# Performance work log

Measured on AMD Instinct MI355X. Metric: run time of the kernel, lower is better.

## Reference

```python
import jax, jax.numpy as jnp
import numpy as np

M, K, N = 8192, 1024, 8192

def setup_inputs() -> dict:
    key = jax.random.key(0)
    k1, k2, k3, k4 = jax.random.split(key, 4)
    # a, b are int8-valued quantized tensors (stored as int32 per harness dtype set)
    a = jax.random.randint(k1, (M, K), 0, 127, dtype=jnp.int32)
    b = jax.random.randint(k2, (K, N), 0, 127, dtype=jnp.int32)
    alpha_row = jax.random.uniform(k3, (M, 1), dtype=jnp.float32)
    alpha_col = jax.random.uniform(k4, (1, N), dtype=jnp.float32)
    return {"a": a, "b": b, "alpha_row": alpha_row, "alpha_col": alpha_col}

def reference(a, b, alpha_row, alpha_col):
    # Faithful to TorchGemmA8W8.forward: upcast int8 operands to fp32,
    # matmul with fp32 accumulate, cast result to int8.
    # (alpha_row / alpha_col are accepted but unused in this variant.)
    x = jnp.matmul(a.astype(jnp.float32), b.astype(jnp.float32))  # [M, N] fp32
    return x.astype(jnp.int8)
```

## Files before the change

kernel.cpp:

```cpp
#include <hip/hip_runtime.h>
#include <stdint.h>

#define M_DIM 8192
#define N_DIM 8192
#define K_DIM 1024
#define BK    128

typedef int int4v __attribute__((ext_vector_type(4)));

__device__ __forceinline__ void gload16(const char* g, char* l) {
    __builtin_amdgcn_global_load_lds(
        (__attribute__((address_space(1))) void*)(void*)const_cast<char*>(g),
        (__attribute__((address_space(3))) void*)l,
        16, 0, 0);
}

__device__ __forceinline__ int sat8(int v) {
    v = v > 127 ? 127 : v;
    v = v < -128 ? -128 : v;
    return v;
}

__global__ __launch_bounds__(256) void pack_ab_kernel(const int* __restrict__ a,
                                                      const int* __restrict__ b,
                                                      char* __restrict__ outA,
                                                      char* __restrict__ outB) {
    __shared__ char tile[64][68];
    const int t = threadIdx.x;
    if (blockIdx.x < 8192) {
        const int m   = blockIdx.x;
        const int row = m & 127;
        const int xr  = (row >> 1) & 3;
        const int4 v  = ((const int4*)a)[m * 256 + t];
        const int pk  = (v.x & 0xff) | ((v.y & 0xff) << 8) |
                        ((v.z & 0xff) << 16) | ((v.w & 0xff) << 24);
        const int k     = t * 4;
        const int slice = k >> 6;
        const int sc    = ((k >> 4) & 3) ^ xr;
        *(int*)&outA[(size_t)(m >> 7) * 131072 + slice * 8192 + row * 64 +
                     sc * 16 + (k & 15)] = pk;
        return;
    }
    const int bx = blockIdx.x - 8192;
    const int n0 = (bx & 127) * 64;
    const int k0 = (bx >> 7) * 64;
    const int tr  = t >> 4;
    const int tc4 = (t & 15) << 2;
#pragma unroll
    for (int j = 0; j < 4; ++j) {
        int row = tr + j * 16;
        int4 v = *(const int4*)&b[(size_t)(k0 + row) * N_DIM + n0 + tc4];
        tile[row][tc4 + 0] = (char)v.x;
        tile[row][tc4 + 1] = (char)v.y;
        tile[row][tc4 + 2] = (char)v.z;
        tile[row][tc4 + 3] = (char)v.w;
    }
    __syncthreads();
    const int slice = k0 >> 6;
#pragma unroll
    for (int j = 0; j < 4; ++j) {
        int n = tr + j * 16;
        int pk = (tile[tc4 + 0][n] & 0xff) |
                 ((tile[tc4 + 1][n] & 0xff) << 8) |
                 ((tile[tc4 + 2][n] & 0xff) << 16) |
                 ((tile[tc4 + 3][n] & 0xff) << 24);
        const int ng  = n0 + n;
        const int row = ng & 127;
        const int sc  = (tc4 >> 4) ^ ((row >> 1) & 3);
        *(int*)&outB[(size_t)(ng >> 7) * 131072 + slice * 8192 + row * 64 +
                     sc * 16 + (tc4 & 15)] = pk;
    }
}

__global__ __launch_bounds__(256) void gemm_i8_kernel(const char* __restrict__ A8,
                                                      const char* __restrict__ B8,
                                                      int* __restrict__ C) {
    __shared__ __align__(16) char smem[4 * 8704];
    char* As = smem;
    char* Bs = smem + 16384;

    const int t    = threadIdx.x;
    const int xcd  = blockIdx.x & 7;
    const int j    = blockIdx.x >> 3;
    const int bm   = (xcd << 3) | (j & 7);
    const int bn   = j >> 3;
    const int lane = t & 63;
    const int wave = t >> 6;
    const int wm   = wave >> 1;
    const int wn   = wave & 1;
    const int quad = lane >> 4;
    const int l16  = lane & 15;

    const char* aT = A8 + (size_t)bm * 131072;
    const char* bT = B8 + (size_t)bn * 131072;

    const int laneByte = ((quad ^ ((l16 >> 1) & 3)) << 4);

    int4v acc[4][4] = {};

    for (int kt = 0; kt < K_DIM / BK; ++kt) {
        const size_t kBase = (size_t)kt * 16384;
#pragma unroll
        for (int s = 0; s < 4; ++s) {
            const int f = s * 4096 + t * 16;
            gload16(aT + kBase + f, As + f);
            gload16(bT + kBase + f, Bs + f);
        }
        __syncthreads();

#pragma unroll
        for (int h = 0; h < 2; ++h) {
            int4v af[4], bf[4];
#pragma unroll
            for (int mi = 0; mi < 4; ++mi)
                af[mi] = *(const int4v*)
                    &As[h * 8192 + (wm * 64 + mi * 16 + l16) * 64 + laneByte];
#pragma unroll
            for (int ni = 0; ni < 4; ++ni)
                bf[ni] = *(const int4v*)
                    &Bs[h * 8192 + (wn * 64 + ni * 16 + l16) * 64 + laneByte];

#pragma unroll
            for (int mi = 0; mi < 4; ++mi)
#pragma unroll
                for (int ni = 0; ni < 4; ++ni)
                    acc[mi][ni] = __builtin_amdgcn_mfma_i32_16x16x64_i8(
                        af[mi], bf[ni], acc[mi][ni], 0, 0, 0);
        }

        __syncthreads();
    }

    int* lw = (int*)(smem + wave * 8704);
    const int mW = bm * 128 + wm * 64;
    const int nW = bn * 128 + wn * 64;
#pragma unroll
    for (int rnd = 0; rnd < 2; ++rnd) {
#pragma unroll
        for (int mh = 0; mh < 2; ++mh) {
            const int mi = rnd * 2 + mh;
#pragma unroll
            for (int ni = 0; ni < 4; ++ni)
#pragma unroll
                for (int r = 0; r < 4; ++r)
                    lw[(mh * 16 + quad * 4 + r) * 68 + ni * 16 + l16] =
                        sat8(acc[mi][ni][r]);
        }
#pragma unroll
        for (int rr = 0; rr < 8; ++rr) {
            const int R = rr * 4 + quad;
            const int4v v = *(const int4v*)&lw[R * 68 + l16 * 4];
            *(int4v*)&C[(size_t)(mW + rnd * 32 + R) * N_DIM + nW + l16 * 4] = v;
        }
    }
}

__global__ __launch_bounds__(256) void gemm_naive_kernel(const int* __restrict__ a,
                                                         const int* __restrict__ b,
                                                         int* __restrict__ C) {
    const int col = blockIdx.x * 256 + threadIdx.x;
    const int row = blockIdx.y;
    int acc = 0;
    for (int k = 0; k < K_DIM; ++k)
        acc += a[(size_t)row * K_DIM + k] * b[(size_t)k * N_DIM + col];
    C[(size_t)row * N_DIM + col] = sat8(acc);
}

extern "C" void kernel_launch(void* const* d_in, const int* in_sizes, int n_in,
                              void* d_out, int out_size, void* d_ws, size_t ws_size,
                              hipStream_t stream) {
    const int* a = (const int*)d_in[0];
    const int* b = (const int*)d_in[1];
    int* out = (int*)d_out;

    const size_t needed = 2 * (size_t)M_DIM * K_DIM;
    if (ws_size < needed) {
        gemm_naive_kernel<<<dim3(N_DIM / 256, M_DIM), 256, 0, stream>>>(a, b, out);
        return;
    }

    char* A8 = (char*)d_ws;
    char* B8 = A8 + (size_t)M_DIM * K_DIM;

    pack_ab_kernel<<<8192 + 2048, 256, 0, stream>>>(a, b, A8, B8);
    gemm_i8_kernel<<<4096, 256, 0, stream>>>(A8, B8, out);
}
```

Baseline: 366.7 us.

## Use 256x256 tiles with a four-slot LDS ring and phase-interleaved prefetch

The int8 GEMM kernel moves from 128x128 tiles with 256 threads to 256x256 tiles with 512 threads, so each wave computes a 128x64 output block and reuses more data per LDS load. Staging becomes a four-slot ring of 64-deep k slices. Each MFMA phase issues one async global-to-LDS copy for a later slice, guarded by explicit barriers, waitcnt and setprio, so global loads overlap compute instead of stalling on a sync per k tile. In exchange, the kernel uses 128 KB of LDS (about one block per CU), drops the XCD-aware block remapping, and carries many more accumulator registers.

```diff
diff --git a/kernel.cpp b/kernel.cpp
--- a/kernel.cpp
+++ b/kernel.cpp
@@ -4,7 +4,6 @@
 #define M_DIM 8192
 #define N_DIM 8192
 #define K_DIM 1024
-#define BK    128
 
 typedef int int4v __attribute__((ext_vector_type(4)));
 
@@ -72,70 +71,103 @@
     }
 }
 
-__global__ __launch_bounds__(256) void gemm_i8_kernel(const char* __restrict__ A8,
-                                                      const char* __restrict__ B8,
-                                                      int* __restrict__ C) {
-    __shared__ __align__(16) char smem[4 * 8704];
-    char* As = smem;
-    char* Bs = smem + 16384;
+__global__ __launch_bounds__(512, 2) void gemm_i8_kernel(const char* __restrict__ A8,
+                                                         const char* __restrict__ B8,
+                                                         int* __restrict__ C) {
+    __shared__ __align__(16) char smem[131072];
 
     const int t    = threadIdx.x;
-    const int xcd  = blockIdx.x & 7;
-    const int j    = blockIdx.x >> 3;
-    const int bm   = (xcd << 3) | (j & 7);
-    const int bn   = j >> 3;
+    const int bn   = blockIdx.x;
+    const int bm   = blockIdx.y;
     const int lane = t & 63;
     const int wave = t >> 6;
-    const int wm   = wave >> 1;
-    const int wn   = wave & 1;
+    const int wm   = wave >> 2;
+    const int wn   = wave & 3;
     const int quad = lane >> 4;
     const int l16  = lane & 15;
-
-    const char* aT = A8 + (size_t)bm * 131072;
-    const char* bT = B8 + (size_t)bn * 131072;
+    const int f16  = t * 16;
+
+    const char* aT0 = A8 + (size_t)(2 * bm) * 131072;
+    const char* aT1 = aT0 + 131072;
+    const char* bT0 = B8 + (size_t)(2 * bn) * 131072;
+    const char* bT1 = bT0 + 131072;
 
     const int laneByte = ((quad ^ ((l16 >> 1) & 3)) << 4);
-
-    int4v acc[4][4] = {};
-
-    for (int kt = 0; kt < K_DIM / BK; ++kt) {
-        const size_t kBase = (size_t)kt * 16384;
-#pragma unroll
-        for (int s = 0; s < 4; ++s) {
-            const int f = s * 4096 + t * 16;
-            gload16(aT + kBase + f, As + f);
-            gload16(bT + kBase + f, Bs + f);
-        }
-        __syncthreads();
-
-#pragma unroll
-        for (int h = 0; h < 2; ++h) {
-            int4v af[4], bf[4];
-#pragma unroll
-            for (int mi = 0; mi < 4; ++mi)
-                af[mi] = *(const int4v*)
-                    &As[h * 8192 + (wm * 64 + mi * 16 + l16) * 64 + laneByte];
-#pragma unroll
-            for (int ni = 0; ni < 4; ++ni)
-                bf[ni] = *(const int4v*)
-                    &Bs[h * 8192 + (wn * 64 + ni * 16 + l16) * 64 + laneByte];
-
-#pragma unroll
-            for (int mi = 0; mi < 4; ++mi)
-#pragma unroll
-                for (int ni = 0; ni < 4; ++ni)
-                    acc[mi][ni] = __builtin_amdgcn_mfma_i32_16x16x64_i8(
-                        af[mi], bf[ni], acc[mi][ni], 0, 0, 0);
-        }
-
-        __syncthreads();
-    }
+    const int aRowByte = (wm * 128 + l16) * 64 + laneByte;
+    const int bRowByte = (wn * 64 + l16) * 64 + laneByte;
+
+    int4v acc[8][4] = {};
+    int4v bf[4];
+
+#define STG_A0(T,S) gload16(aT0 + (T)*8192 + f16, smem + (S)*16384 + f16)
+#define STG_A1(T,S) gload16(aT1 + (T)*8192 + f16, smem + (S)*16384 + 8192 + f16)
+#define STG_B0(T,S) gload16(bT0 + (T)*8192 + f16, smem + 65536 + (S)*16384 + f16)
+#define STG_B1(T,S) gload16(bT1 + (T)*8192 + f16, smem + 65536 + (S)*16384 + 8192 + f16)
+
+#define PHASE(SLOT, MIH, LOADB, STG, VMW) do {                                      \
+    int4v af0 = *(const int4v*)&smem[(SLOT)*16384 + aRowByte + ((MIH)*2+0)*1024];   \
+    int4v af1 = *(const int4v*)&smem[(SLOT)*16384 + aRowByte + ((MIH)*2+1)*1024];   \
+    if (LOADB) {                                                                    \
+        bf[0] = *(const int4v*)&smem[65536 + (SLOT)*16384 + bRowByte + 0*1024];     \
+        bf[1] = *(const int4v*)&smem[65536 + (SLOT)*16384 + bRowByte + 1*1024];     \
+        bf[2] = *(const int4v*)&smem[65536 + (SLOT)*16384 + bRowByte + 2*1024];     \
+        bf[3] = *(const int4v*)&smem[65536 + (SLOT)*16384 + bRowByte + 3*1024];     \
+    }                                                                               \
+    STG;                                                                            \
+    __builtin_amdgcn_s_barrier();                                                   \
+    asm volatile("s_waitcnt lgkmcnt(0)" ::: "memory");                              \
+    __builtin_amdgcn_sched_barrier(0);                                 \
+    __builtin_amdgcn_s_setprio(1);                                                  \
+    _Pragma("unroll")                                                               \
+    for (int ni = 0; ni < 4; ++ni) {                                                \
+        acc[(MIH)*2+0][ni] = __builtin_amdgcn_mfma_i32_16x16x64_i8(                 \
+            af0, bf[ni], acc[(MIH)*2+0][ni], 0, 0, 0);                              \
+        acc[(MIH)*2+1][ni] = __builtin_amdgcn_mfma_i32_16x16x64_i8(                 \
+            af1, bf[ni], acc[(MIH)*2+1][ni], 0, 0, 0);                              \
+    }                                                                               \
+    __builtin_amdgcn_s_setprio(0);                                                  \
+    if (VMW) asm volatile("s_waitcnt vmcnt(4)" ::: "memory");                       \
+    __builtin_amdgcn_s_barrier();                                                   \
+} while (0)
+
+    STG_A0(0, 0); STG_A1(0, 0); STG_B0(0, 0); STG_B1(0, 0);
+    STG_A0(1, 1); STG_A1(1, 1); STG_B0(1, 1); STG_B1(1, 1);
+    asm volatile("s_waitcnt vmcnt(4)" ::: "memory");
+    __builtin_amdgcn_s_barrier();
+    __builtin_amdgcn_sched_barrier(0);
+
+#pragma unroll 2
+    for (int j = 0; j < 8; ++j) {
+        const int s0 = (2 * j) & 3;
+        const int s1 = (2 * j + 1) & 3;
+        const int su0 = (2 * j + 2) & 3;
+        const int su1 = (2 * j + 3) & 3;
+        const int u0 = (j < 7) ? 2 * j + 2 : 15;
+        const int u1 = (j < 7) ? 2 * j + 3 : 15;
+
+        PHASE(s0, 0, 1, STG_A0(u0, su0), 0);
+        PHASE(s0, 1, 0, STG_A1(u0, su0), 0);
+        PHASE(s0, 2, 0, STG_B0(u0, su0), 0);
+        PHASE(s0, 3, 0, STG_B1(u0, su0), 1);
+        PHASE(s1, 0, 1, STG_A0(u1, su1), 0);
+        PHASE(s1, 1, 0, STG_A1(u1, su1), 0);
+        PHASE(s1, 2, 0, STG_B0(u1, su1), 0);
+        PHASE(s1, 3, 0, STG_B1(u1, su1), 1);
+    }
+#undef PHASE
+#undef STG_A0
+#undef STG_A1
+#undef STG_B0
+#undef STG_B1
+
+    asm volatile("s_waitcnt vmcnt(0)" ::: "memory");
+    __builtin_amdgcn_s_barrier();
 
     int* lw = (int*)(smem + wave * 8704);
-    const int mW = bm * 128 + wm * 64;
-    const int nW = bn * 128 + wn * 64;
-#pragma unroll
-    for (int rnd = 0; rnd < 2; ++rnd) {
+    const int mBase = bm * 256 + wm * 128;
+    const int nW    = bn * 256 + wn * 64;
+#pragma unroll
+    for (int rnd = 0; rnd < 4; ++rnd) {
 #pragma unroll
         for (int mh = 0; mh < 2; ++mh) {
             const int mi = rnd * 2 + mh;
@@ -150,7 +182,7 @@
         for (int rr = 0; rr < 8; ++rr) {
             const int R = rr * 4 + quad;
             const int4v v = *(const int4v*)&lw[R * 68 + l16 * 4];
-            *(int4v*)&C[(size_t)(mW + rnd * 32 + R) * N_DIM + nW + l16 * 4] = v;
+            *(int4v*)&C[(size_t)(mBase + rnd * 32 + R) * N_DIM + nW + l16 * 4] = v;
         }
     }
 }
@@ -183,5 +215,5 @@
     char* B8 = A8 + (size_t)M_DIM * K_DIM;
 
     pack_ab_kernel<<<8192 + 2048, 256, 0, stream>>>(a, b, A8, B8);
-    gemm_i8_kernel<<<4096, 256, 0, stream>>>(A8, B8, out);
-}
+    gemm_i8_kernel<<<dim3(N_DIM / 256, M_DIM / 256), 512, 0, stream>>>(A8, B8, out);
+}
```

Measured after the change: 367.8 us. No clear change (+0.3%).

## Give each wave private double-buffered LDS tiles and drop block barriers

Applied to the files above, without the earlier changes.

The shared block-wide tile load with two __syncthreads per K step is replaced by per-wave private LDS regions. Each wave streams only its own 64-row A and B slices through a two-deep buffer using global_load_lds, synchronising with explicit vmcnt/lgkmcnt waits and raising priority around the MFMA block. This removes the barriers and overlaps the global loads with compute. The cost is redundant global traffic, since waves sharing a row or column each fetch the same slice, and the tail re-issues dummy loads of the last slice.

```diff
diff --git a/kernel.cpp b/kernel.cpp
--- a/kernel.cpp
+++ b/kernel.cpp
@@ -4,7 +4,6 @@
 #define M_DIM 8192
 #define N_DIM 8192
 #define K_DIM 1024
-#define BK    128
 
 typedef int int4v __attribute__((ext_vector_type(4)));
 
@@ -75,9 +74,7 @@
 __global__ __launch_bounds__(256) void gemm_i8_kernel(const char* __restrict__ A8,
                                                       const char* __restrict__ B8,
                                                       int* __restrict__ C) {
-    __shared__ __align__(16) char smem[4 * 8704];
-    char* As = smem;
-    char* Bs = smem + 16384;
+    __shared__ __align__(16) char smem[4][16384];
 
     const int t    = threadIdx.x;
     const int xcd  = blockIdx.x & 7;
@@ -90,48 +87,71 @@
     const int wn   = wave & 1;
     const int quad = lane >> 4;
     const int l16  = lane & 15;
-
-    const char* aT = A8 + (size_t)bm * 131072;
-    const char* bT = B8 + (size_t)bn * 131072;
+    const int lb   = lane * 16;
+
+    char* myA = &smem[wave][0];
+    char* myB = &smem[wave][8192];
+
+    const char* aW = A8 + (size_t)bm * 131072 + wm * 4096;
+    const char* bW = B8 + (size_t)bn * 131072 + wn * 4096;
 
     const int laneByte = ((quad ^ ((l16 >> 1) & 3)) << 4);
 
     int4v acc[4][4] = {};
 
-    for (int kt = 0; kt < K_DIM / BK; ++kt) {
-        const size_t kBase = (size_t)kt * 16384;
-#pragma unroll
-        for (int s = 0; s < 4; ++s) {
-            const int f = s * 4096 + t * 16;
-            gload16(aT + kBase + f, As + f);
-            gload16(bT + kBase + f, Bs + f);
-        }
-        __syncthreads();
-
-#pragma unroll
-        for (int h = 0; h < 2; ++h) {
-            int4v af[4], bf[4];
-#pragma unroll
-            for (int mi = 0; mi < 4; ++mi)
-                af[mi] = *(const int4v*)
-                    &As[h * 8192 + (wm * 64 + mi * 16 + l16) * 64 + laneByte];
+#define STG(SL, BUF) do {                                                     \
+    const char* as_ = aW + (SL) * 8192;                                       \
+    const char* bs_ = bW + (SL) * 8192;                                       \
+    char* la_ = myA + (BUF) * 4096;                                           \
+    char* lb_ = myB + (BUF) * 4096;                                           \
+    gload16(as_ + lb,        la_ + lb);                                       \
+    gload16(as_ + 1024 + lb, la_ + 1024 + lb);                                \
+    gload16(as_ + 2048 + lb, la_ + 2048 + lb);                                \
+    gload16(as_ + 3072 + lb, la_ + 3072 + lb);                                \
+    gload16(bs_ + lb,        lb_ + lb);                                       \
+    gload16(bs_ + 1024 + lb, lb_ + 1024 + lb);                                \
+    gload16(bs_ + 2048 + lb, lb_ + 2048 + lb);                                \
+    gload16(bs_ + 3072 + lb, lb_ + 3072 + lb);                                \
+} while (0)
+
+    STG(0, 0);
+    STG(1, 1);
+
+#pragma unroll 2
+    for (int kt = 0; kt < 16; ++kt) {
+        const int buf = kt & 1;
+        asm volatile("s_waitcnt vmcnt(8)" ::: "memory");
+        __builtin_amdgcn_sched_barrier(0);
+
+        int4v af[4], bf[4];
+#pragma unroll
+        for (int mi = 0; mi < 4; ++mi)
+            af[mi] = *(const int4v*)
+                &myA[buf * 4096 + (mi * 16 + l16) * 64 + laneByte];
+#pragma unroll
+        for (int ni = 0; ni < 4; ++ni)
+            bf[ni] = *(const int4v*)
+                &myB[buf * 4096 + (ni * 16 + l16) * 64 + laneByte];
+
+        asm volatile("s_waitcnt lgkmcnt(0)" ::: "memory");
+        __builtin_amdgcn_sched_barrier(0);
+
+        STG((kt + 2 < 16) ? kt + 2 : 15, buf);
+
+        __builtin_amdgcn_s_setprio(1);
+#pragma unroll
+        for (int mi = 0; mi < 4; ++mi)
 #pragma unroll
             for (int ni = 0; ni < 4; ++ni)
-                bf[ni] = *(const int4v*)
-                    &Bs[h * 8192 + (wn * 64 + ni * 16 + l16) * 64 + laneByte];
-
-#pragma unroll
-            for (int mi = 0; mi < 4; ++mi)
-#pragma unroll
-                for (int ni = 0; ni < 4; ++ni)
-                    acc[mi][ni] = __builtin_amdgcn_mfma_i32_16x16x64_i8(
-                        af[mi], bf[ni], acc[mi][ni], 0, 0, 0);
-        }
-
-        __syncthreads();
-    }
-
-    int* lw = (int*)(smem + wave * 8704);
+                acc[mi][ni] = __builtin_amdgcn_mfma_i32_16x16x64_i8(
+                    af[mi], bf[ni], acc[mi][ni], 0, 0, 0);
+        __builtin_amdgcn_s_setprio(0);
+    }
+#undef STG
+
+    asm volatile("s_waitcnt vmcnt(0)" ::: "memory");
+
+    int* lw = (int*)&smem[wave][0];
     const int mW = bm * 128 + wm * 64;
     const int nW = bn * 128 + wn * 64;
 #pragma unroll
```

Result: slower. 382.7 us (+4.4%).
